# Kernel optimization log

Measured on AMD Instinct MI355X. Metric: run time of the kernel, lower is better.

The kernel has to match this reference:

```python
import jax, jax.numpy as jnp
import numpy as np

IN_FEATURES = 4096
OUT_FEATURES = 11008
BATCH = 16


def setup_inputs() -> dict:
    key = jax.random.key(0)
    k_x, k_w, k_s, k_b = jax.random.split(key, 4)
    x = jax.random.normal(k_x, (BATCH, IN_FEATURES), dtype=jnp.float32)
    # symmetric int8 weights stored as int32 for jax portability (values in [-127, 127])
    weight_int8 = jax.random.randint(k_w, (OUT_FEATURES, IN_FEATURES), -127, 128, dtype=jnp.int32)
    # per-output-channel scales, small positive values typical of int8 quantization
    weight_scale = jax.random.uniform(k_s, (OUT_FEATURES,), dtype=jnp.float32, minval=0.005, maxval=0.02)
    bias = jax.random.normal(k_b, (OUT_FEATURES,), dtype=jnp.float32)
    return {"x": x, "weight_int8": weight_int8, "weight_scale": weight_scale, "bias": bias}


def reference(x, weight_int8, weight_scale, bias):
    # Dequantize: w_dq[o, i] = int8[o, i] * scale[o]  -> fp32 [OUT, IN]
    w_dq = weight_int8.astype(x.dtype) * weight_scale[:, None]
    # F.linear: y = x @ w_dq.T + bias  -> [BATCH, OUT]
    return jnp.einsum("bi,oi->bo", x, w_dq) + bias
```

## Files before the change

### kernel.cpp

```cpp
#include <hip/hip_runtime.h>

#define IN_F   4096
#define OUT_F  11008
#define BATCH  16
#define CO     16
#define BLOCK  256
#define SPLITK 8
#define KCHUNK (IN_F / SPLITK)

typedef int i32x4 __attribute__((ext_vector_type(4)));

__global__ __launch_bounds__(BLOCK) void init_out_kernel(
    const float* __restrict__ bias, float* __restrict__ out)
{
    int idx = blockIdx.x * BLOCK + threadIdx.x;
    if (idx < BATCH * OUT_F) {
        int o = idx % OUT_F;
        out[idx] = bias[o];
    }
}

__global__ __launch_bounds__(BLOCK) void qlin_kernel(
    const float* __restrict__ x,
    const int*   __restrict__ w,
    const float* __restrict__ scale,
    float* __restrict__ out)
{
    __shared__ float xs[BATCH][KCHUNK];

    const int tid = threadIdx.x;
    const int tx  = tid & 63;
    const int ty  = tid >> 6;
    const int o0  = blockIdx.x * CO + ty * 4;
    const int kb  = blockIdx.y * KCHUNK;

    const i32x4* __restrict__ wbase = (const i32x4*)(w + (size_t)o0 * IN_F);

    i32x4 wv[2][4];
    #pragma unroll
    for (int it = 0; it < 2; ++it) {
        const size_t kg4 = (size_t)((kb >> 2) + it * 64 + tx);
        #pragma unroll
        for (int r = 0; r < 4; ++r)
            wv[it][r] = __builtin_nontemporal_load(wbase + kg4 + (size_t)r * (IN_F / 4));
    }

    #pragma unroll
    for (int j = 0; j < (BATCH * KCHUNK / 4) / BLOCK; ++j) {
        int f  = tid + j * BLOCK;
        int b  = f >> 7;
        int kc = f & 127;
        const float* src = x + (size_t)b * IN_F + kb + kc * 4;
        void* dst = (char*)&xs[0][0] + (size_t)f * 16;
        __builtin_amdgcn_global_load_lds(
            (const __attribute__((address_space(1))) void*)src,
            (__attribute__((address_space(3))) void*)dst,
            16, 0, 0);
    }

    __syncthreads();

    float acc[64];
    #pragma unroll
    for (int i = 0; i < 64; ++i) acc[i] = 0.f;

    #pragma unroll
    for (int it = 0; it < 2; ++it) {
        const int kl = it * 256 + tx * 4;

        float wf[4][4];
        #pragma unroll
        for (int r = 0; r < 4; ++r)
            #pragma unroll
            for (int e = 0; e < 4; ++e)
                wf[r][e] = (float)wv[it][r][e];

        #pragma unroll
        for (int bc = 0; bc < 4; ++bc) {
            float4 xv[4];
            #pragma unroll
            for (int bb = 0; bb < 4; ++bb)
                xv[bb] = *(const float4*)&xs[bc * 4 + bb][kl];

            #pragma unroll
            for (int r = 0; r < 4; ++r)
                #pragma unroll
                for (int bb = 0; bb < 4; ++bb) {
                    float a = acc[r * 16 + bc * 4 + bb];
                    a += wf[r][0] * xv[bb].x;
                    a += wf[r][1] * xv[bb].y;
                    a += wf[r][2] * xv[bb].z;
                    a += wf[r][3] * xv[bb].w;
                    acc[r * 16 + bc * 4 + bb] = a;
                }
        }
    }

    #pragma unroll
    for (int wd = 32; wd >= 1; wd >>= 1) {
        const bool upper = (tx & wd) != 0;
        #pragma unroll
        for (int i = 0; i < wd; ++i) {
            float lo = acc[i]      + __shfl_xor(acc[i],      wd);
            float hi = acc[i + wd] + __shfl_xor(acc[i + wd], wd);
            acc[i] = upper ? hi : lo;
        }
    }

    const int o = o0 + (tx >> 4);
    const int b = tx & 15;
    atomicAdd(&out[(size_t)b * OUT_F + o], acc[0] * scale[o]);
}

extern "C" void kernel_launch(void* const* d_in, const int* in_sizes, int n_in,
                              void* d_out, int out_size, void* d_ws, size_t ws_size,
                              hipStream_t stream) {
    const float* x     = (const float*)d_in[0];
    const int*   w     = (const int*)d_in[1];
    const float* scale = (const float*)d_in[2];
    const float* bias  = (const float*)d_in[3];
    float* out = (float*)d_out;

    init_out_kernel<<<(BATCH * OUT_F + BLOCK - 1) / BLOCK, BLOCK, 0, stream>>>(bias, out);

    dim3 grid(OUT_F / CO, SPLITK);
    qlin_kernel<<<grid, dim3(BLOCK), 0, stream>>>(x, w, scale, out);
}
```

Baseline: 266.7 us.

## Compute int8 GEMV with bf16 MFMA using split hi/lo activations

Replaces the scalar FMA inner loop with 16x16x32 bf16 MFMA instructions. Activations are split into bf16 high and low parts so two MFMAs keep near-fp32 accuracy, and the int weights are exactly representable in bf16. Each wave now covers 16 output rows over the block's K chunk, with software double-buffered weight loads and padded LDS. It drops the nontemporal hint and the cross-lane shuffle reduction. The kernel is bound by reading the int32 weights from memory, so the compute savings may matter less than the changed load pattern.

```diff
diff --git a/kernel.cpp b/kernel.cpp
--- a/kernel.cpp
+++ b/kernel.cpp
@@ -3,12 +3,16 @@
 #define IN_F   4096
 #define OUT_F  11008
 #define BATCH  16
-#define CO     16
 #define BLOCK  256
 #define SPLITK 8
 #define KCHUNK (IN_F / SPLITK)
+#define XPAD   8
+#define XSTRIDE (KCHUNK + XPAD)
+#define NSTEP  (KCHUNK / 32)
 
-typedef int i32x4 __attribute__((ext_vector_type(4)));
+typedef short s16x8 __attribute__((ext_vector_type(8)));
+typedef float f32x4 __attribute__((ext_vector_type(4)));
+typedef int   i32x4 __attribute__((ext_vector_type(4)));
 
 __global__ __launch_bounds__(BLOCK) void init_out_kernel(
     const float* __restrict__ bias, float* __restrict__ out)
@@ -20,96 +24,88 @@
     }
 }
 
+__device__ __forceinline__ unsigned short bf16_trunc_bits(float f) {
+    return (unsigned short)(__float_as_uint(f) >> 16);
+}
+
 __global__ __launch_bounds__(BLOCK) void qlin_kernel(
     const float* __restrict__ x,
     const int*   __restrict__ w,
     const float* __restrict__ scale,
     float* __restrict__ out)
 {
-    __shared__ float xs[BATCH][KCHUNK];
+    __shared__ alignas(16) unsigned short xhi[BATCH * XSTRIDE];
+    __shared__ alignas(16) unsigned short xlo[BATCH * XSTRIDE];
 
-    const int tid = threadIdx.x;
-    const int tx  = tid & 63;
-    const int ty  = tid >> 6;
-    const int o0  = blockIdx.x * CO + ty * 4;
-    const int kb  = blockIdx.y * KCHUNK;
+    const int tid  = threadIdx.x;
+    const int lane = tid & 63;
+    const int wv   = tid >> 6;
+    const int n    = lane & 15;
+    const int quad = lane >> 4;
+    const int o0   = blockIdx.x * 64 + wv * 16;
+    const int kb   = blockIdx.y * KCHUNK;
 
-    const i32x4* __restrict__ wbase = (const i32x4*)(w + (size_t)o0 * IN_F);
-
-    i32x4 wv[2][4];
-    #pragma unroll
-    for (int it = 0; it < 2; ++it) {
-        const size_t kg4 = (size_t)((kb >> 2) + it * 64 + tx);
-        #pragma unroll
-        for (int r = 0; r < 4; ++r)
-            wv[it][r] = __builtin_nontemporal_load(wbase + kg4 + (size_t)r * (IN_F / 4));
-    }
-
+    const float4* __restrict__ xg = (const float4*)x;
     #pragma unroll
     for (int j = 0; j < (BATCH * KCHUNK / 4) / BLOCK; ++j) {
         int f  = tid + j * BLOCK;
         int b  = f >> 7;
         int kc = f & 127;
-        const float* src = x + (size_t)b * IN_F + kb + kc * 4;
-        void* dst = (char*)&xs[0][0] + (size_t)f * 16;
-        __builtin_amdgcn_global_load_lds(
-            (const __attribute__((address_space(1))) void*)src,
-            (__attribute__((address_space(3))) void*)dst,
-            16, 0, 0);
+        float4 v = xg[(size_t)b * (IN_F / 4) + (kb >> 2) + kc];
+        ushort4 h, l;
+        {
+            unsigned u;
+            u = __float_as_uint(v.x); h.x = u >> 16;
+            l.x = bf16_trunc_bits(v.x - __uint_as_float(u & 0xFFFF0000u));
+            u = __float_as_uint(v.y); h.y = u >> 16;
+            l.y = bf16_trunc_bits(v.y - __uint_as_float(u & 0xFFFF0000u));
+            u = __float_as_uint(v.z); h.z = u >> 16;
+            l.z = bf16_trunc_bits(v.z - __uint_as_float(u & 0xFFFF0000u));
+            u = __float_as_uint(v.w); h.w = u >> 16;
+            l.w = bf16_trunc_bits(v.w - __uint_as_float(u & 0xFFFF0000u));
+        }
+        *(ushort4*)&xhi[b * XSTRIDE + kc * 4] = h;
+        *(ushort4*)&xlo[b * XSTRIDE + kc * 4] = l;
+    }
+    __syncthreads();
+
+    const int* __restrict__ wrow = w + (size_t)(o0 + n) * IN_F + kb + quad * 8;
+    i32x4 wa[2], wb[2];
+    wa[0] = *(const i32x4*)(wrow);
+    wb[0] = *(const i32x4*)(wrow + 4);
+
+    f32x4 acc = {0.f, 0.f, 0.f, 0.f};
+
+    #pragma unroll
+    for (int s = 0; s < NSTEP; ++s) {
+        const int cur = s & 1, nxt = cur ^ 1;
+        if (s + 1 < NSTEP) {
+            wa[nxt] = *(const i32x4*)(wrow + (s + 1) * 32);
+            wb[nxt] = *(const i32x4*)(wrow + (s + 1) * 32 + 4);
+        }
+
+        s16x8 bfrag;
+        #pragma unroll
+        for (int e = 0; e < 4; ++e) {
+            bfrag[e]     = (short)bf16_trunc_bits((float)wa[cur][e]);
+            bfrag[4 + e] = (short)bf16_trunc_bits((float)wb[cur][e]);
+        }
+
+        const int xoff = n * XSTRIDE + s * 32 + quad * 8;
+        s16x8 ah = *(const s16x8*)&xhi[xoff];
+        s16x8 al = *(const s16x8*)&xlo[xoff];
+
+        acc = __builtin_amdgcn_mfma_f32_16x16x32_bf16(ah, bfrag, acc, 0, 0, 0);
+        acc = __builtin_amdgcn_mfma_f32_16x16x32_bf16(al, bfrag, acc, 0, 0, 0);
     }
 
-    __syncthreads();
-
-    float acc[64];
+    const int   o  = o0 + n;
+    const float sc = scale[o];
     #pragma unroll
-    for (int i = 0; i < 64; ++i) acc[i] = 0.f;
-
-    #pragma unroll
-    for (int it = 0; it < 2; ++it) {
-        const int kl = it * 256 + tx * 4;
-
-        float wf[4][4];
-        #pragma unroll
-        for (int r = 0; r < 4; ++r)
-            #pragma unroll
-            for (int e = 0; e < 4; ++e)
-                wf[r][e] = (float)wv[it][r][e];
-
-        #pragma unroll
-        for (int bc = 0; bc < 4; ++bc) {
-            float4 xv[4];
-            #pragma unroll
-            for (int bb = 0; bb < 4; ++bb)
-                xv[bb] = *(const float4*)&xs[bc * 4 + bb][kl];
-
-            #pragma unroll
-            for (int r = 0; r < 4; ++r)
-                #pragma unroll
-                for (int bb = 0; bb < 4; ++bb) {
-                    float a = acc[r * 16 + bc * 4 + bb];
-                    a += wf[r][0] * xv[bb].x;
-                    a += wf[r][1] * xv[bb].y;
-                    a += wf[r][2] * xv[bb].z;
-                    a += wf[r][3] * xv[bb].w;
-                    acc[r * 16 + bc * 4 + bb] = a;
-                }
-        }
+    for (int r = 0; r < 4; ++r) {
+        const int b = quad * 4 + r;
+        atomicAdd(&out[(size_t)b * OUT_F + o], acc[r] * sc);
     }
-
-    #pragma unroll
-    for (int wd = 32; wd >= 1; wd >>= 1) {
-        const bool upper = (tx & wd) != 0;
-        #pragma unroll
-        for (int i = 0; i < wd; ++i) {
-            float lo = acc[i]      + __shfl_xor(acc[i],      wd);
-            float hi = acc[i + wd] + __shfl_xor(acc[i + wd], wd);
-            acc[i] = upper ? hi : lo;
-        }
-    }
-
-    const int o = o0 + (tx >> 4);
-    const int b = tx & 15;
-    atomicAdd(&out[(size_t)b * OUT_F + o], acc[0] * scale[o]);
 }
 
 extern "C" void kernel_launch(void* const* d_in, const int* in_sizes, int n_in,
@@ -123,6 +119,6 @@
 
     init_out_kernel<<<(BATCH * OUT_F + BLOCK - 1) / BLOCK, BLOCK, 0, stream>>>(bias, out);
 
-    dim3 grid(OUT_F / CO, SPLITK);
+    dim3 grid(OUT_F / 64, SPLITK);
     qlin_kernel<<<grid, dim3(BLOCK), 0, stream>>>(x, w, scale, out);
 }
```

After: 261.8 us. No clear change (-1.8%).
